# Kernel tuning notes

Hardware: AMD Instinct MI355X
Metric: run time of the kernel (lower is better)

Reference implementation:

```python
import jax, jax.numpy as jnp
import numpy as np

B, V, C = 8192, 512, 16  # batch, num_variables, constraints per variable
N1 = V + 1  # augmented with bias column


def setup_inputs() -> dict:
    key = jax.random.key(0)
    k1, k2, k3 = jax.random.split(key, 3)
    preds = jax.random.normal(k1, (B, V), dtype=jnp.float32)
    # Acyclic structure: variable v's constraints only reference earlier
    # variables (columns < v) plus the bias column (column V).
    cols = jnp.arange(N1)[None, :]              # [1, N1]
    vids = jnp.arange(V)[:, None]               # [V, 1]
    mask = ((cols < vids) | (cols == V)).astype(jnp.float32)[:, None, :]  # [V,1,N1]
    scale = 0.1
    pos_mats = jax.random.normal(k2, (V, C, N1), dtype=jnp.float32) * scale * mask
    neg_mats = jax.random.normal(k3, (V, C, N1), dtype=jnp.float32) * scale * mask
    return {"preds": preds, "pos_mats": pos_mats, "neg_mats": neg_mats}


def reference(preds, pos_mats, neg_mats):
    # Augment preds with a ones column (bias), as in the original __call__.
    b = preds.shape[0]
    p0 = jnp.concatenate([preds, jnp.ones((b, 1), preds.dtype)], axis=1)  # [B, N1]
    var_ids = jnp.arange(pos_mats.shape[0])

    def step(p, xs):
        pm, nm, v = xs  # pm, nm: [C, N1]
        # apply_matrix: (preds * matrix).sum(-1) with max / min reduction over C
        lower = jnp.einsum('bn,cn->bc', p, pm).max(axis=1)  # [B]
        upper = jnp.einsum('bn,cn->bc', p, nm).min(axis=1)  # [B]
        # get_final_x_correction: clamp prediction into [lower, upper]
        corrected = jnp.minimum(jnp.maximum(p[:, v], lower), upper)
        p = p.at[:, v].set(corrected)
        return p, None

    pf, _ = jax.lax.scan(step, p0, (pos_mats, neg_mats, var_ids))
    return pf[:, : preds.shape[1]]
```

## Files before the change

kernel.cpp:

```cpp
#include <hip/hip_runtime.h>

#define BATCH 8192
#define V 512
#define N1 513
#define KCH 16
#define NCHUNKS 32
#define RB 32
#define NT 1024
#define PKS 520
#define SJP 772

typedef __bf16 bf16_t;
typedef bf16_t bf16x8 __attribute__((ext_vector_type(8)));
typedef float f32x4 __attribute__((ext_vector_type(4)));
typedef float f32x2 __attribute__((ext_vector_type(2)));

#define EPP 4194304ull
#define DV_OFF (EPP * 2ull)
#define BV_OFF (DV_OFF + 1048576ull)

__device__ __forceinline__ f32x4 mfma16(bf16x8 a, bf16x8 b, f32x4 c) {
    return __builtin_amdgcn_mfma_f32_16x16x32_bf16(a, b, c, 0, 0, 0);
}

__device__ __forceinline__ float bcast_lane(float x, int l) {
    return __int_as_float(__builtin_amdgcn_readlane(__float_as_int(x), l));
}

__device__ __forceinline__ float dpp_xor1_max(float x) {
    const int xi = __float_as_int(x);
    const float o = __int_as_float(
        __builtin_amdgcn_update_dpp(xi, xi, 0xB1, 0xF, 0xF, false));
    return fmaxf(x, o);
}

__global__ __launch_bounds__(1024)
void repack_all(const float* __restrict__ pos, const float* __restrict__ neg,
                bf16_t* __restrict__ Mhi, float* __restrict__ Dv,
                float* __restrict__ Bv)
{
    __shared__ float sb[2 * 256 * 36];
    const int bx  = blockIdx.x;
    const int tid = threadIdx.x;
    if (bx < 496) {
        const int cc  = (bx >> 4) + 1;
        const int kb  = bx & 15;
        const int nkb = (cc + 1) >> 1;
        if (kb >= nkb) return;
        const int klen = 16 * cc;
        for (int idx = tid; idx < 8192; idx += 1024) {
            const int r = idx >> 5, k32 = idx & 31;
            const int k = kb * 32 + k32;
            const size_t row = (size_t)cc * 256 + r;
            float xp = 0.0f, xn = 0.0f;
            if (k < klen) {
                xp = pos[row * N1 + k];
                xn = -neg[row * N1 + k];
            }
            sb[r * 36 + k32]            = xp;
            sb[256 * 36 + r * 36 + k32] = xn;
        }
        __syncthreads();
        const size_t base = 16384ull * (size_t)((cc * cc) / 4) + (size_t)kb * 16384ull;
        for (int e8 = tid; e8 < 2048; e8 += 1024) {
            const int t = e8 >> 6, s = e8 & 63;
            const int c = s & 15, q = s >> 4;
            const int vloc = t >> 1, m = t & 1;
            const float* sp = &sb[m * 256 * 36 + (vloc * 16 + c) * 36 + 8 * q];
            bf16x8 o;
            #pragma unroll
            for (int jj = 0; jj < 8; ++jj) o[jj] = (bf16_t)sp[jj];
            *(bf16x8*)(Mhi + base + (size_t)e8 * 8) = o;
        }
    } else {
        const int cc = bx - 496;
        float* bufP = sb;
        float* bufN = sb + 256 * 17;
        for (int idx = tid; idx < 4096; idx += 1024) {
            const int r = idx >> 4, kk = idx & 15;
            const size_t row = (size_t)(cc * 256 + r);
            bufP[r * 17 + kk] = pos[row * N1 + cc * 16 + kk];
            bufN[r * 17 + kk] = neg[row * N1 + cc * 16 + kk];
        }
        __syncthreads();
        for (int idx = tid; idx < 8192; idx += 1024) {
            const int vl = idx >> 9, j = idx & 511;
            const int vlo = j >> 5, c = j & 15;
            const int m = (j >> 4) & 1;
            const float x = (m ? bufN : bufP)[(vlo * 16 + c) * 17 + vl];
            Dv[(size_t)cc * 8192 + idx] = m ? -x : x;
        }
        for (int j = tid; j < 512; j += 1024) {
            const int vlo = j >> 5, c = j & 15;
            const int m = (j >> 4) & 1;
            const float* src = m ? neg : pos;
            const float x = src[(size_t)(cc * 256 + vlo * 16 + c) * N1 + V];
            Bv[(size_t)cc * 512 + j] = m ? -x : x;
        }
    }
}

__global__ __launch_bounds__(NT, 4)
void shield_fused(const float* __restrict__ preds,
                  const bf16_t* __restrict__ Mhi,
                  const float* __restrict__ Dv, const float* __restrict__ Bv,
                  float* __restrict__ out)
{
    __shared__ bf16_t Phi[RB * PKS];
    __shared__ float  S[RB * SJP];

    const int tid  = threadIdx.x;
    const int b0   = blockIdx.x * RB;
    const int lane = tid & 63;
    const int w    = tid >> 6;
    const int cq   = lane & 15;
    const int q    = lane >> 4;
    const int rp0  = w * 2;

    {
        const int r = tid >> 5, seg = tid & 31;
        const float* prow = preds + (size_t)(b0 + r) * V + seg * 16;
        #pragma unroll
        for (int k = 0; k < 16; k += 4) {
            const float4 p4 = *(const float4*)(prow + k);
            const int n = seg * 16 + k;
            Phi[r * PKS + n + 0] = (bf16_t)p4.x;
            Phi[r * PKS + n + 1] = (bf16_t)p4.y;
            Phi[r * PKS + n + 2] = (bf16_t)p4.z;
            Phi[r * PKS + n + 3] = (bf16_t)p4.w;
        }
    }

    int tJ[2], sct[2];
    #pragma unroll
    for (int tt = 0; tt < 2; ++tt) {
        tJ[tt]  = ((2 * w + tt) << 4) + cq;
        sct[tt] = 12 * (tJ[tt] >> 3) + (tJ[tt] & 7);
    }
    const int aoff0 = cq * PKS + 8 * q;
    const int aoff1 = (16 + cq) * PKS + 8 * q;

    f32x4 acc[2][2];
    #pragma unroll
    for (int tt = 0; tt < 2; ++tt) {
        const float b = Bv[tJ[tt]];
        acc[0][tt] = f32x4{b, b, b, b};
        acc[1][tt] = f32x4{b, b, b, b};
    }

    #pragma unroll 1
    for (int cc = 0; cc < NCHUNKS; ++cc) {
        const int v0 = cc * 16;
        const int  ccn  = cc + 1;
        const bool hasN = ccn < NCHUNKS;
        const int  nkbN = hasN ? ((ccn + 1) >> 1) : 0;
        const bf16_t* phN = Mhi + 16384ull * (size_t)((ccn * ccn) / 4)
                          + (size_t)lane * 8 + (size_t)(2 * w) * 512;

        #pragma unroll
        for (int tt = 0; tt < 2; ++tt)
            #pragma unroll
            for (int reg = 0; reg < 4; ++reg) {
                S[(4 * q + reg) * SJP + sct[tt]]      = acc[0][tt][reg];
                S[(16 + 4 * q + reg) * SJP + sct[tt]] = acc[1][tt][reg];
            }
        __syncthreads();

        f32x2 s2[8];
        {
            const float* sp = &S[rp0 * SJP + 12 * lane];
            const float4 a0 = *(const float4*)(sp);
            const float4 a1 = *(const float4*)(sp + 4);
            const float4 c0 = *(const float4*)(sp + SJP);
            const float4 c1 = *(const float4*)(sp + SJP + 4);
            s2[0] = f32x2{a0.x, c0.x}; s2[1] = f32x2{a0.y, c0.y};
            s2[2] = f32x2{a0.z, c0.z}; s2[3] = f32x2{a0.w, c0.w};
            s2[4] = f32x2{a1.x, c1.x}; s2[5] = f32x2{a1.y, c1.y};
            s2[6] = f32x2{a1.z, c1.z}; s2[7] = f32x2{a1.w, c1.w};
        }

        const bf16x8 poA0 = *(const bf16x8*)(Phi + rp0 * PKS + v0);
        const bf16x8 poA1 = *(const bf16x8*)(Phi + rp0 * PKS + v0 + 8);
        const bf16x8 poB0 = *(const bf16x8*)(Phi + (rp0 + 1) * PKS + v0);
        const bf16x8 poB1 = *(const bf16x8*)(Phi + (rp0 + 1) * PKS + v0 + 8);

        if (hasN) {
            #pragma unroll
            for (int tt = 0; tt < 2; ++tt) {
                const float b = Bv[(ccn << 9) + tJ[tt]];
                acc[0][tt] = f32x4{b, b, b, b};
                acc[1][tt] = f32x4{b, b, b, b};
            }
        }

        #pragma unroll
        for (int vl = 0; vl < KCH; ++vl) {
            const int vcur = v0 + vl;
            const bool doKb = hasN && (vl < nkbN - 1);

            bf16x8 fa0, fa1, fb0, fb1;
            if (doKb) {
                const int k0 = vl * 32;
                fa0 = *(const bf16x8*)(Phi + aoff0 + k0);
                fa1 = *(const bf16x8*)(Phi + aoff1 + k0);
                const bf16_t* pb = phN + (size_t)k0 * 512;
                fb0 = *(const bf16x8*)(pb);
                fb1 = *(const bf16x8*)(pb + 512);
            }

            float dv[8];
            {
                const float* dp = Dv + ((size_t)vcur << 9) + 8 * lane;
                const float4 d0 = *(const float4*)(dp);
                const float4 d1 = *(const float4*)(dp + 4);
                dv[0]=d0.x; dv[1]=d0.y; dv[2]=d0.z; dv[3]=d0.w;
                dv[4]=d1.x; dv[5]=d1.y; dv[6]=d1.z; dv[7]=d1.w;
            }
            const float po_[2] = {
                (float)(vl < 8 ? poA0[vl & 7] : poA1[vl & 7]),
                (float)(vl < 8 ? poB0[vl & 7] : poB1[vl & 7])
            };

            float red[2];
            #pragma unroll
            for (int r = 0; r < 2; ++r) {
                const float m0 = fmaxf(fmaxf(s2[0][r], s2[1][r]), s2[2][r]);
                const float m1 = fmaxf(fmaxf(s2[3][r], s2[4][r]), s2[5][r]);
                const float m2 = fmaxf(s2[6][r], s2[7][r]);
                const float mxr = fmaxf(fmaxf(m0, m1), m2);
                red[r] = dpp_xor1_max(mxr);
            }
            float pc[2];
            #pragma unroll
            for (int r = 0; r < 2; ++r) {
                const float lw  = bcast_lane(red[r], 4 * vl);
                const float nup = bcast_lane(red[r], 4 * vl + 2);
                pc[r] = fminf(fmaxf(po_[r], lw), -nup);
            }
            if (lane == 4 * vl) {
                Phi[rp0 * PKS + vcur]       = (bf16_t)pc[0];
                Phi[(rp0 + 1) * PKS + vcur] = (bf16_t)pc[1];
            }
            const f32x2 pcv = {pc[0], pc[1]};
            #pragma unroll
            for (int jj = 0; jj < 8; ++jj) {
                const f32x2 dsp = {dv[jj], dv[jj]};
                s2[jj] = __builtin_elementwise_fma(dsp, pcv, s2[jj]);
            }

            if (doKb) {
                acc[0][0] = mfma16(fa0, fb0, acc[0][0]);
                acc[1][0] = mfma16(fa1, fb0, acc[1][0]);
                acc[0][1] = mfma16(fa0, fb1, acc[0][1]);
                acc[1][1] = mfma16(fa1, fb1, acc[1][1]);
            }
        }

        __syncthreads();

        if (hasN) {
            const int k0 = (nkbN - 1) * 32;
            const bf16x8 fa0 = *(const bf16x8*)(Phi + aoff0 + k0);
            const bf16x8 fa1 = *(const bf16x8*)(Phi + aoff1 + k0);
            const bf16_t* pb = phN + (size_t)k0 * 512;
            const bf16x8 fb0 = *(const bf16x8*)(pb);
            const bf16x8 fb1 = *(const bf16x8*)(pb + 512);
            acc[0][0] = mfma16(fa0, fb0, acc[0][0]);
            acc[1][0] = mfma16(fa1, fb0, acc[1][0]);
            acc[0][1] = mfma16(fa0, fb1, acc[0][1]);
            acc[1][1] = mfma16(fa1, fb1, acc[1][1]);
        }
    }

    {
        const int r = tid >> 5, seg = tid & 31;
        float* orow = out + (size_t)(b0 + r) * V + seg * 16;
        #pragma unroll
        for (int k = 0; k < 16; k += 4) {
            const int n = seg * 16 + k;
            float4 o;
            o.x = (float)Phi[r * PKS + n + 0];
            o.y = (float)Phi[r * PKS + n + 1];
            o.z = (float)Phi[r * PKS + n + 2];
            o.w = (float)Phi[r * PKS + n + 3];
            *(float4*)(orow + k) = o;
        }
    }
}

extern "C" void kernel_launch(void* const* d_in, const int* in_sizes, int n_in,
                              void* d_out, int out_size, void* d_ws, size_t ws_size,
                              hipStream_t stream) {
    const float* preds = (const float*)d_in[0];
    const float* pos   = (const float*)d_in[1];
    const float* neg   = (const float*)d_in[2];
    float* o = (float*)d_out;
    char* base = (char*)d_ws;
    bf16_t* Mhi = (bf16_t*)base;
    float*  Dv  = (float*)(base + DV_OFF);
    float*  Bv  = (float*)(base + BV_OFF);
    repack_all<<<dim3(528), 1024, 0, stream>>>(pos, neg, Mhi, Dv, Bv);
    shield_fused<<<dim3(BATCH / RB), NT, 0, stream>>>(preds, Mhi, Dv, Bv, o);
}
```

Measured before the change: 380.0 us.

## Halve rows per block to one row per wave and raise occupancy

Drops the per-block batch tile from 32 to 16 rows, so each wave owns one batch row instead of two. The intra-chunk sequential clamp loop now works on scalars rather than packed pairs, and the lookahead MFMA for the next chunk's partial products needs two instructions per step instead of four. Shared memory per block shrinks and launch bounds request 8 blocks per CU, trading per-wave ILP and B-operand reuse for more resident blocks and twice as many workgroups. Dv and Mhi are now read twice as often per output row.

Result: slower. 456.4 us (+20.1%).

```diff
diff --git a/kernel.cpp b/kernel.cpp
--- a/kernel.cpp
+++ b/kernel.cpp
@@ -5,15 +5,14 @@
 #define N1 513
 #define KCH 16
 #define NCHUNKS 32
-#define RB 32
+#define RB 16
 #define NT 1024
 #define PKS 520
-#define SJP 772
+#define SJ2 516
 
 typedef __bf16 bf16_t;
 typedef bf16_t bf16x8 __attribute__((ext_vector_type(8)));
 typedef float f32x4 __attribute__((ext_vector_type(4)));
-typedef float f32x2 __attribute__((ext_vector_type(2)));
 
 #define EPP 4194304ull
 #define DV_OFF (EPP * 2ull)
@@ -100,14 +99,14 @@
     }
 }
 
-__global__ __launch_bounds__(NT, 4)
+__global__ __launch_bounds__(NT, 8)
 void shield_fused(const float* __restrict__ preds,
                   const bf16_t* __restrict__ Mhi,
                   const float* __restrict__ Dv, const float* __restrict__ Bv,
                   float* __restrict__ out)
 {
     __shared__ bf16_t Phi[RB * PKS];
-    __shared__ float  S[RB * SJP];
+    __shared__ float  S[RB * SJ2];
 
     const int tid  = threadIdx.x;
     const int b0   = blockIdx.x * RB;
@@ -115,37 +114,32 @@
     const int w    = tid >> 6;
     const int cq   = lane & 15;
     const int q    = lane >> 4;
-    const int rp0  = w * 2;
 
     {
-        const int r = tid >> 5, seg = tid & 31;
-        const float* prow = preds + (size_t)(b0 + r) * V + seg * 16;
-        #pragma unroll
-        for (int k = 0; k < 16; k += 4) {
-            const float4 p4 = *(const float4*)(prow + k);
-            const int n = seg * 16 + k;
-            Phi[r * PKS + n + 0] = (bf16_t)p4.x;
-            Phi[r * PKS + n + 1] = (bf16_t)p4.y;
-            Phi[r * PKS + n + 2] = (bf16_t)p4.z;
-            Phi[r * PKS + n + 3] = (bf16_t)p4.w;
-        }
-    }
-
-    int tJ[2], sct[2];
+        const float* prow = preds + (size_t)(b0 + w) * V + lane * 8;
+        const float4 p0 = *(const float4*)(prow);
+        const float4 p1 = *(const float4*)(prow + 4);
+        const int n = lane * 8;
+        Phi[w * PKS + n + 0] = (bf16_t)p0.x;
+        Phi[w * PKS + n + 1] = (bf16_t)p0.y;
+        Phi[w * PKS + n + 2] = (bf16_t)p0.z;
+        Phi[w * PKS + n + 3] = (bf16_t)p0.w;
+        Phi[w * PKS + n + 4] = (bf16_t)p1.x;
+        Phi[w * PKS + n + 5] = (bf16_t)p1.y;
+        Phi[w * PKS + n + 6] = (bf16_t)p1.z;
+        Phi[w * PKS + n + 7] = (bf16_t)p1.w;
+    }
+
+    int tJ[2];
     #pragma unroll
-    for (int tt = 0; tt < 2; ++tt) {
-        tJ[tt]  = ((2 * w + tt) << 4) + cq;
-        sct[tt] = 12 * (tJ[tt] >> 3) + (tJ[tt] & 7);
-    }
-    const int aoff0 = cq * PKS + 8 * q;
-    const int aoff1 = (16 + cq) * PKS + 8 * q;
-
-    f32x4 acc[2][2];
+    for (int tt = 0; tt < 2; ++tt) tJ[tt] = ((2 * w + tt) << 4) + cq;
+    const int aoff = cq * PKS + 8 * q;
+
+    f32x4 acc[2];
     #pragma unroll
     for (int tt = 0; tt < 2; ++tt) {
         const float b = Bv[tJ[tt]];
-        acc[0][tt] = f32x4{b, b, b, b};
-        acc[1][tt] = f32x4{b, b, b, b};
+        acc[tt] = f32x4{b, b, b, b};
     }
 
     #pragma unroll 1
@@ -160,36 +154,24 @@
         #pragma unroll
         for (int tt = 0; tt < 2; ++tt)
             #pragma unroll
-            for (int reg = 0; reg < 4; ++reg) {
-                S[(4 * q + reg) * SJP + sct[tt]]      = acc[0][tt][reg];
-                S[(16 + 4 * q + reg) * SJP + sct[tt]] = acc[1][tt][reg];
-            }
-        __syncthreads();
-
-        f32x2 s2[8];
+            for (int reg = 0; reg < 4; ++reg)
+                S[(4 * q + reg) * SJ2 + tJ[tt]] = acc[tt][reg];
+        __syncthreads();
+
+        float s2[8];
         {
-            const float* sp = &S[rp0 * SJP + 12 * lane];
+            const float* sp = &S[w * SJ2 + 8 * lane];
             const float4 a0 = *(const float4*)(sp);
             const float4 a1 = *(const float4*)(sp + 4);
-            const float4 c0 = *(const float4*)(sp + SJP);
-            const float4 c1 = *(const float4*)(sp + SJP + 4);
-            s2[0] = f32x2{a0.x, c0.x}; s2[1] = f32x2{a0.y, c0.y};
-            s2[2] = f32x2{a0.z, c0.z}; s2[3] = f32x2{a0.w, c0.w};
-            s2[4] = f32x2{a1.x, c1.x}; s2[5] = f32x2{a1.y, c1.y};
-            s2[6] = f32x2{a1.z, c1.z}; s2[7] = f32x2{a1.w, c1.w};
-        }
-
-        const bf16x8 poA0 = *(const bf16x8*)(Phi + rp0 * PKS + v0);
-        const bf16x8 poA1 = *(const bf16x8*)(Phi + rp0 * PKS + v0 + 8);
-        const bf16x8 poB0 = *(const bf16x8*)(Phi + (rp0 + 1) * PKS + v0);
-        const bf16x8 poB1 = *(const bf16x8*)(Phi + (rp0 + 1) * PKS + v0 + 8);
+            s2[0] = a0.x; s2[1] = a0.y; s2[2] = a0.z; s2[3] = a0.w;
+            s2[4] = a1.x; s2[5] = a1.y; s2[6] = a1.z; s2[7] = a1.w;
+        }
 
         if (hasN) {
             #pragma unroll
             for (int tt = 0; tt < 2; ++tt) {
                 const float b = Bv[(ccn << 9) + tJ[tt]];
-                acc[0][tt] = f32x4{b, b, b, b};
-                acc[1][tt] = f32x4{b, b, b, b};
+                acc[tt] = f32x4{b, b, b, b};
             }
         }
 
@@ -198,11 +180,10 @@
             const int vcur = v0 + vl;
             const bool doKb = hasN && (vl < nkbN - 1);
 
-            bf16x8 fa0, fa1, fb0, fb1;
+            bf16x8 fa, fb0, fb1;
             if (doKb) {
                 const int k0 = vl * 32;
-                fa0 = *(const bf16x8*)(Phi + aoff0 + k0);
-                fa1 = *(const bf16x8*)(Phi + aoff1 + k0);
+                fa  = *(const bf16x8*)(Phi + aoff + k0);
                 const bf16_t* pb = phN + (size_t)k0 * 512;
                 fb0 = *(const bf16x8*)(pb);
                 fb1 = *(const bf16x8*)(pb + 512);
@@ -216,43 +197,23 @@
                 dv[0]=d0.x; dv[1]=d0.y; dv[2]=d0.z; dv[3]=d0.w;
                 dv[4]=d1.x; dv[5]=d1.y; dv[6]=d1.z; dv[7]=d1.w;
             }
-            const float po_[2] = {
-                (float)(vl < 8 ? poA0[vl & 7] : poA1[vl & 7]),
-                (float)(vl < 8 ? poB0[vl & 7] : poB1[vl & 7])
-            };
-
-            float red[2];
-            #pragma unroll
-            for (int r = 0; r < 2; ++r) {
-                const float m0 = fmaxf(fmaxf(s2[0][r], s2[1][r]), s2[2][r]);
-                const float m1 = fmaxf(fmaxf(s2[3][r], s2[4][r]), s2[5][r]);
-                const float m2 = fmaxf(s2[6][r], s2[7][r]);
-                const float mxr = fmaxf(fmaxf(m0, m1), m2);
-                red[r] = dpp_xor1_max(mxr);
-            }
-            float pc[2];
-            #pragma unroll
-            for (int r = 0; r < 2; ++r) {
-                const float lw  = bcast_lane(red[r], 4 * vl);
-                const float nup = bcast_lane(red[r], 4 * vl + 2);
-                pc[r] = fminf(fmaxf(po_[r], lw), -nup);
-            }
-            if (lane == 4 * vl) {
-                Phi[rp0 * PKS + vcur]       = (bf16_t)pc[0];
-                Phi[(rp0 + 1) * PKS + vcur] = (bf16_t)pc[1];
-            }
-            const f32x2 pcv = {pc[0], pc[1]};
-            #pragma unroll
-            for (int jj = 0; jj < 8; ++jj) {
-                const f32x2 dsp = {dv[jj], dv[jj]};
-                s2[jj] = __builtin_elementwise_fma(dsp, pcv, s2[jj]);
-            }
+            const float po = (float)Phi[w * PKS + vcur];
+
+            const float m0 = fmaxf(fmaxf(s2[0], s2[1]), s2[2]);
+            const float m1 = fmaxf(fmaxf(s2[3], s2[4]), s2[5]);
+            const float m2 = fmaxf(s2[6], s2[7]);
+            const float red = dpp_xor1_max(fmaxf(fmaxf(m0, m1), m2));
+            const float lw  = bcast_lane(red, 4 * vl);
+            const float nup = bcast_lane(red, 4 * vl + 2);
+            const float pc  = fminf(fmaxf(po, lw), -nup);
+            if (lane == 4 * vl) Phi[w * PKS + vcur] = (bf16_t)pc;
+
+            #pragma unroll
+            for (int jj = 0; jj < 8; ++jj) s2[jj] = fmaf(dv[jj], pc, s2[jj]);
 
             if (doKb) {
-                acc[0][0] = mfma16(fa0, fb0, acc[0][0]);
-                acc[1][0] = mfma16(fa1, fb0, acc[1][0]);
-                acc[0][1] = mfma16(fa0, fb1, acc[0][1]);
-                acc[1][1] = mfma16(fa1, fb1, acc[1][1]);
+                acc[0] = mfma16(fa, fb0, acc[0]);
+                acc[1] = mfma16(fa, fb1, acc[1]);
             }
         }
 
@@ -260,31 +221,29 @@
 
         if (hasN) {
             const int k0 = (nkbN - 1) * 32;
-            const bf16x8 fa0 = *(const bf16x8*)(Phi + aoff0 + k0);
-            const bf16x8 fa1 = *(const bf16x8*)(Phi + aoff1 + k0);
+            const bf16x8 fa  = *(const bf16x8*)(Phi + aoff + k0);
             const bf16_t* pb = phN + (size_t)k0 * 512;
             const bf16x8 fb0 = *(const bf16x8*)(pb);
             const bf16x8 fb1 = *(const bf16x8*)(pb + 512);
-            acc[0][0] = mfma16(fa0, fb0, acc[0][0]);
-            acc[1][0] = mfma16(fa1, fb0, acc[1][0]);
-            acc[0][1] = mfma16(fa0, fb1, acc[0][1]);
-            acc[1][1] = mfma16(fa1, fb1, acc[1][1]);
+            acc[0] = mfma16(fa, fb0, acc[0]);
+            acc[1] = mfma16(fa, fb1, acc[1]);
         }
     }
 
     {
-        const int r = tid >> 5, seg = tid & 31;
-        float* orow = out + (size_t)(b0 + r) * V + seg * 16;
-        #pragma unroll
-        for (int k = 0; k < 16; k += 4) {
-            const int n = seg * 16 + k;
-            float4 o;
-            o.x = (float)Phi[r * PKS + n + 0];
-            o.y = (float)Phi[r * PKS + n + 1];
-            o.z = (float)Phi[r * PKS + n + 2];
-            o.w = (float)Phi[r * PKS + n + 3];
-            *(float4*)(orow + k) = o;
-        }
+        float* orow = out + (size_t)(b0 + w) * V + lane * 8;
+        const int n = lane * 8;
+        float4 o0, o1;
+        o0.x = (float)Phi[w * PKS + n + 0];
+        o0.y = (float)Phi[w * PKS + n + 1];
+        o0.z = (float)Phi[w * PKS + n + 2];
+        o0.w = (float)Phi[w * PKS + n + 3];
+        o1.x = (float)Phi[w * PKS + n + 4];
+        o1.y = (float)Phi[w * PKS + n + 5];
+        o1.z = (float)Phi[w * PKS + n + 6];
+        o1.w = (float)Phi[w * PKS + n + 7];
+        *(float4*)(orow)     = o0;
+        *(float4*)(orow + 4) = o1;
     }
 }
 
```
